# Optimization experiments

Measured on AMD Instinct MI355X. Metric: run time of the kernel, lower is better.

Reference implementation:

```python
import jax, jax.numpy as jnp
import numpy as np

TEMPERATURE = 0.5
EPS = 1e-8  # torch.nn.CosineSimilarity eps


def _l2norm(x):
    # torch cosine sim divides by max(||x||, eps) per vector
    n = jnp.sqrt(jnp.sum(x * x, axis=-1, keepdims=True))
    return x / jnp.maximum(n, EPS)


def setup_inputs() -> dict:
    key = jax.random.key(0)
    ka, kb = jax.random.split(key)
    batch_a = jax.random.normal(ka, (4096, 512), dtype=jnp.float32)
    batch_b = jax.random.normal(kb, (4096, 512), dtype=jnp.float32)
    return {"batch_a": batch_a, "batch_b": batch_b}


def reference(batch_a, batch_b):
    a = _l2norm(batch_a)  # [N, D]
    b = _l2norm(batch_b)
    inv_t = 1.0 / TEMPERATURE
    # cosine similarity via normalize + GEMM (same math as broadcast mul+reduce)
    sim11 = (a @ a.T) * inv_t  # [N, N]
    sim22 = (b @ b.T) * inv_t
    sim12 = (a @ b.T) * inv_t
    n = sim12.shape[-1]
    eye = jnp.eye(n, dtype=bool)
    neg_inf = jnp.float32(-jnp.inf)
    sim11 = jnp.where(eye, neg_inf, sim11)
    sim22 = jnp.where(eye, neg_inf, sim22)
    # logits: [[sim12, sim11], [sim22, sim12^T]] -> [2N, 2N]
    logits = jnp.concatenate(
        [jnp.concatenate([sim12, sim11], axis=-1),
         jnp.concatenate([sim22, sim12.T], axis=-1)],
        axis=-2,
    )
    targets = jnp.arange(2 * n)
    logp = jax.nn.log_softmax(logits, axis=-1)  # stable single pass
    loss = -jnp.mean(logp[jnp.arange(2 * n), targets])
    return loss
```

## Files before the change

### kernel.cpp

```cpp
#include <hip/hip_runtime.h>

#define NR 4096
#define DD 512
#define TWO_N 8192
#define MT2 32
#define NT2 528
#define CH2 66

using bf16x8 = __attribute__((ext_vector_type(8))) short;
using f32x4  = __attribute__((ext_vector_type(4))) float;

__device__ __forceinline__ unsigned short f2bf(float f) {
    union { float f; unsigned u; } v; v.f = f;
    unsigned r = v.u + 0x7fff + ((v.u >> 16) & 1);
    return (unsigned short)(r >> 16);
}

__global__ __launch_bounds__(256) void ntx_nrm_kernel(const float* __restrict__ A,
                                                      const float* __restrict__ B,
                                                      unsigned short* __restrict__ X,
                                                      float* __restrict__ d12,
                                                      float* __restrict__ S) {
    const int row = blockIdx.x;
    const int t = threadIdx.x;
    const int lane = t & 63, wid = t >> 6;

    if (t < 2) S[row * 2 + t] = 0.f;

    const float2 av = *(const float2*)(A + row * DD + 2 * t);
    const float2 bv = *(const float2*)(B + row * DD + 2 * t);
    float sa = av.x * av.x + av.y * av.y;
    float sb = bv.x * bv.x + bv.y * bv.y;
#pragma unroll
    for (int o = 32; o; o >>= 1) { sa += __shfl_down(sa, o); sb += __shfl_down(sb, o); }

    __shared__ float red[12];
    if (lane == 0) { red[wid] = sa; red[4 + wid] = sb; }
    __syncthreads();
    const float ta = red[0] + red[1] + red[2] + red[3];
    const float tb = red[4] + red[5] + red[6] + red[7];
    const float ra = 1.f / fmaxf(sqrtf(ta), 1e-8f);
    const float rb = 1.f / fmaxf(sqrtf(tb), 1e-8f);
    const float nax = av.x * ra, nay = av.y * ra;
    const float nbx = bv.x * rb, nby = bv.y * rb;

    *(unsigned*)(X + row * DD + 2 * t) =
        (unsigned)f2bf(nax) | ((unsigned)f2bf(nay) << 16);
    *(unsigned*)(X + (NR + row) * DD + 2 * t) =
        (unsigned)f2bf(nbx) | ((unsigned)f2bf(nby) << 16);

    float dt = nax * nbx + nay * nby;
#pragma unroll
    for (int o = 32; o; o >>= 1) dt += __shfl_down(dt, o);
    if (lane == 0) red[8 + wid] = dt;
    __syncthreads();
    if (t == 0) d12[row] = red[8] + red[9] + red[10] + red[11];
}

__global__ __launch_bounds__(512, 1) void ntx_gemm_lse_kernel(const unsigned short* __restrict__ X,
                                                              float* __restrict__ S) {
    const int bid = blockIdx.x;
    const int sid = (bid & 7) * CH2 + (bid >> 3);
    int u, v;
    if (sid < 448) {
        const int s = sid >> 4, loc = sid & 15;
        int U = 0;
        while (7 * (U + 1) - (U + 1) * U / 2 <= s) ++U;
        const int V = U + 1 + (s - (7 * U - U * (U - 1) / 2));
        u = U * 4 + (loc >> 2);
        v = V * 4 + (loc & 3);
    } else {
        const int s2 = sid - 448;
        const int U = s2 / 10, loc = s2 % 10;
        int lu = 0;
        while ((lu + 1) * 4 - (lu + 1) * lu / 2 <= loc) ++lu;
        const int lv = lu + (loc - (lu * 4 - lu * (lu - 1) / 2));
        u = U * 4 + lu;
        v = U * 4 + lv;
    }
    const bool fixedTile = (u == v);
    const int rowTile = u * 256, colTile = (v ^ 16) * 256;

    __shared__ unsigned short As[2][256 * 64];
    __shared__ unsigned short Bs[2][256 * 64];

    const int t = threadIdx.x;
    const int lane = t & 63, wid = t >> 6;
    const int waveM = wid >> 2, waveN = wid & 3;
    const int lr = lane & 15, grp = lane >> 4;
    const int r3 = lr & 7;

    f32x4 acc[8][4] = {};
    bf16x8 af[4][2];
    bf16x8 bf[4][2];

    const int srow = lane >> 3;
    const int scol = ((lane & 7) ^ srow) * 8;

    auto STAGE1 = [&](int sel, int kt, int q) {
        const int ci = wid * 4 + q;
        const int r  = ci * 8 + srow;
        const int lo = ci * 512 + lane * 8;
        __builtin_amdgcn_global_load_lds(
            (const __attribute__((address_space(1))) unsigned*)(X + (size_t)(rowTile + r) * DD + kt + scol),
            (__attribute__((address_space(3))) unsigned*)&As[sel][lo], 16, 0, 0);
        __builtin_amdgcn_global_load_lds(
            (const __attribute__((address_space(1))) unsigned*)(X + (size_t)((colTile + r) ^ NR) * DD + kt + scol),
            (__attribute__((address_space(3))) unsigned*)&Bs[sel][lo], 16, 0, 0);
    };

    auto LDA = [&](int sel, int mh) {
#pragma unroll
        for (int mm = 0; mm < 4; ++mm)
#pragma unroll
            for (int kk = 0; kk < 2; ++kk)
                af[mm][kk] = *(const bf16x8*)&As[sel][(waveM * 128 + (mh * 4 + mm) * 16 + lr) * 64 +
                                                      (((kk * 4 + grp) ^ r3) * 8)];
    };
    auto LDB = [&](int sel, int nh) {
#pragma unroll
        for (int nn = 0; nn < 2; ++nn)
#pragma unroll
            for (int kk = 0; kk < 2; ++kk)
                bf[nh * 2 + nn][kk] = *(const bf16x8*)&Bs[sel][(waveN * 64 + (nh * 2 + nn) * 16 + lr) * 64 +
                                                               (((kk * 4 + grp) ^ r3) * 8)];
    };
    auto QUAD = [&](int mh, int nh) {
        __builtin_amdgcn_s_setprio(1);
#pragma unroll
        for (int mm = 0; mm < 4; ++mm)
#pragma unroll
            for (int nn = 0; nn < 2; ++nn)
#pragma unroll
                for (int kk = 0; kk < 2; ++kk)
                    acc[mh * 4 + mm][nh * 2 + nn] = __builtin_amdgcn_mfma_f32_16x16x32_bf16(
                        af[mm][kk], bf[nh * 2 + nn][kk], acc[mh * 4 + mm][nh * 2 + nn], 0, 0, 0);
        __builtin_amdgcn_s_setprio(0);
    };

    STAGE1(0, 0, 0); STAGE1(0, 0, 1); STAGE1(0, 0, 2); STAGE1(0, 0, 3);
    asm volatile("s_waitcnt vmcnt(0)" ::: "memory");
    __builtin_amdgcn_s_barrier();

    for (int tt = 0; tt < 8; ++tt) {
        const int sel = tt & 1;
        const int kn = (tt + 1) * 64;
        LDA(sel, 0); LDB(sel, 0);
        if (tt < 7) { STAGE1(sel ^ 1, kn, 0); STAGE1(sel ^ 1, kn, 1); }
        __builtin_amdgcn_s_barrier();
        asm volatile("s_waitcnt lgkmcnt(0)" ::: "memory");
        __builtin_amdgcn_sched_barrier(0);
        QUAD(0, 0);
        __builtin_amdgcn_s_barrier();
        LDB(sel, 1);
        if (tt < 7) STAGE1(sel ^ 1, kn, 2);
        __builtin_amdgcn_s_barrier();
        asm volatile("s_waitcnt lgkmcnt(0)" ::: "memory");
        __builtin_amdgcn_sched_barrier(0);
        QUAD(0, 1);
        __builtin_amdgcn_s_barrier();
        LDA(sel, 1);
        if (tt < 7) STAGE1(sel ^ 1, kn, 3);
        __builtin_amdgcn_s_barrier();
        asm volatile("s_waitcnt lgkmcnt(0)" ::: "memory");
        __builtin_amdgcn_sched_barrier(0);
        QUAD(1, 1);
        __builtin_amdgcn_s_barrier();
        QUAD(1, 0);
        if (tt < 7) asm volatile("s_waitcnt vmcnt(0)" ::: "memory");
        __builtin_amdgcn_s_barrier();
    }

#pragma unroll
    for (int m = 0; m < 8; ++m)
#pragma unroll
        for (int n = 0; n < 4; ++n)
#pragma unroll
            for (int reg = 0; reg < 4; ++reg) {
                const int R = rowTile + waveM * 128 + m * 16 + grp * 4 + reg;
                const int C = colTile + waveN * 64 + n * 16 + lr;
                const bool masked = fixedTile && (C == (R ^ NR));
                acc[m][n][reg] = masked ? 0.f : __expf(acc[m][n][reg] * 2.0f);
            }

#pragma unroll
    for (int m = 0; m < 8; ++m)
#pragma unroll
        for (int reg = 0; reg < 4; ++reg) {
            float rs = acc[m][0][reg] + acc[m][1][reg] + acc[m][2][reg] + acc[m][3][reg];
            rs += __shfl_xor(rs, 1);
            rs += __shfl_xor(rs, 2);
            rs += __shfl_xor(rs, 4);
            rs += __shfl_xor(rs, 8);
            if (lr == 0) {
                const int R = rowTile + waveM * 128 + m * 16 + grp * 4 + reg;
                atomicAdd(&S[R], rs);
            }
        }

    if (!fixedTile) {
#pragma unroll
        for (int n = 0; n < 4; ++n) {
            float cs = 0.f;
#pragma unroll
            for (int m = 0; m < 8; ++m)
#pragma unroll
                for (int reg = 0; reg < 4; ++reg)
                    cs += acc[m][n][reg];
            cs += __shfl_xor(cs, 16);
            cs += __shfl_xor(cs, 32);
            if (grp == 0) {
                const int C = colTile + waveN * 64 + n * 16 + lr;
                atomicAdd(&S[C ^ NR], cs);
            }
        }
    }
}

__global__ __launch_bounds__(256) void ntx_loss_kernel(const float* __restrict__ S,
                                                       const float* __restrict__ d12,
                                                       float* __restrict__ out) {
    const int t = threadIdx.x;
    const int r = blockIdx.x * 256 + t;
    float a = __logf(S[r]) - 2.0f * d12[r & (NR - 1)];
    const int lane = t & 63, wid = t >> 6;
#pragma unroll
    for (int o = 32; o; o >>= 1) a += __shfl_down(a, o);
    __shared__ float red[4];
    if (lane == 0) red[wid] = a;
    __syncthreads();
    if (t == 0) atomicAdd(out, (red[0] + red[1] + red[2] + red[3]) * (1.f / (float)TWO_N));
}

extern "C" void kernel_launch(void* const* d_in, const int* in_sizes, int n_in,
                              void* d_out, int out_size, void* d_ws, size_t ws_size,
                              hipStream_t stream) {
    const float* A = (const float*)d_in[0];
    const float* B = (const float*)d_in[1];

    unsigned short* X = (unsigned short*)d_ws;
    float* S   = (float*)((char*)d_ws + (size_t)TWO_N * DD * 2);
    float* d12 = (float*)((char*)S + (size_t)TWO_N * 4);

    hipMemsetAsync(d_out, 0, sizeof(float), stream);

    ntx_nrm_kernel<<<NR, 256, 0, stream>>>(A, B, X, d12, S);

    ntx_gemm_lse_kernel<<<NT2, 512, 0, stream>>>(X, S);

    ntx_loss_kernel<<<TWO_N / 256, 256, 0, stream>>>(S, d12, (float*)d_out);
}
```

Before: 86.87 us.

## Switch GEMM mainloop to triple-buffered K=32 stages with deeper prefetch

The LDS staging in the fused GEMM+LSE kernel moves from double-buffered K=64 tiles to triple-buffered K=32 tiles. Global-to-LDS loads now run two stages ahead, gated by a partial vmcnt wait, and the XOR swizzle is redone for the narrower rows. The goal is to hide global load latency better and cut the per-iteration full vmcnt drain, at the cost of twice as many loop iterations and barriers.

```diff
diff --git a/kernel.cpp b/kernel.cpp
--- a/kernel.cpp
+++ b/kernel.cpp
@@ -81,25 +81,26 @@
     const bool fixedTile = (u == v);
     const int rowTile = u * 256, colTile = (v ^ 16) * 256;
 
-    __shared__ unsigned short As[2][256 * 64];
-    __shared__ unsigned short Bs[2][256 * 64];
+    __shared__ unsigned short As[3][256 * 32];
+    __shared__ unsigned short Bs[3][256 * 32];
 
     const int t = threadIdx.x;
     const int lane = t & 63, wid = t >> 6;
     const int waveM = wid >> 2, waveN = wid & 3;
     const int lr = lane & 15, grp = lane >> 4;
-    const int r3 = lr & 7;
+    const int swr = (lr >> 1) & 3;
+    const int kslot = (grp ^ swr) * 8;
 
     f32x4 acc[8][4] = {};
-    bf16x8 af[4][2];
-    bf16x8 bf[4][2];
-
-    const int srow = lane >> 3;
-    const int scol = ((lane & 7) ^ srow) * 8;
+    bf16x8 af[4];
+    bf16x8 bf[4];
+
+    const int srow = lane >> 2;
+    const int scol = ((lane & 3) ^ ((lane >> 3) & 3)) * 8;
 
     auto STAGE1 = [&](int sel, int kt, int q) {
-        const int ci = wid * 4 + q;
-        const int r  = ci * 8 + srow;
+        const int ci = wid * 2 + q;
+        const int r  = ci * 16 + srow;
         const int lo = ci * 512 + lane * 8;
         __builtin_amdgcn_global_load_lds(
             (const __attribute__((address_space(1))) unsigned*)(X + (size_t)(rowTile + r) * DD + kt + scol),
@@ -112,62 +113,49 @@
     auto LDA = [&](int sel, int mh) {
 #pragma unroll
         for (int mm = 0; mm < 4; ++mm)
-#pragma unroll
-            for (int kk = 0; kk < 2; ++kk)
-                af[mm][kk] = *(const bf16x8*)&As[sel][(waveM * 128 + (mh * 4 + mm) * 16 + lr) * 64 +
-                                                      (((kk * 4 + grp) ^ r3) * 8)];
-    };
-    auto LDB = [&](int sel, int nh) {
-#pragma unroll
-        for (int nn = 0; nn < 2; ++nn)
-#pragma unroll
-            for (int kk = 0; kk < 2; ++kk)
-                bf[nh * 2 + nn][kk] = *(const bf16x8*)&Bs[sel][(waveN * 64 + (nh * 2 + nn) * 16 + lr) * 64 +
-                                                               (((kk * 4 + grp) ^ r3) * 8)];
-    };
-    auto QUAD = [&](int mh, int nh) {
+            af[mm] = *(const bf16x8*)&As[sel][(waveM * 128 + (mh * 4 + mm) * 16 + lr) * 32 + kslot];
+    };
+    auto LDB = [&](int sel) {
+#pragma unroll
+        for (int n = 0; n < 4; ++n)
+            bf[n] = *(const bf16x8*)&Bs[sel][(waveN * 64 + n * 16 + lr) * 32 + kslot];
+    };
+    auto QUAD = [&](int mh) {
         __builtin_amdgcn_s_setprio(1);
 #pragma unroll
         for (int mm = 0; mm < 4; ++mm)
 #pragma unroll
-            for (int nn = 0; nn < 2; ++nn)
-#pragma unroll
-                for (int kk = 0; kk < 2; ++kk)
-                    acc[mh * 4 + mm][nh * 2 + nn] = __builtin_amdgcn_mfma_f32_16x16x32_bf16(
-                        af[mm][kk], bf[nh * 2 + nn][kk], acc[mh * 4 + mm][nh * 2 + nn], 0, 0, 0);
+            for (int n = 0; n < 4; ++n)
+                acc[mh * 4 + mm][n] = __builtin_amdgcn_mfma_f32_16x16x32_bf16(
+                    af[mm], bf[n], acc[mh * 4 + mm][n], 0, 0, 0);
         __builtin_amdgcn_s_setprio(0);
     };
 
-    STAGE1(0, 0, 0); STAGE1(0, 0, 1); STAGE1(0, 0, 2); STAGE1(0, 0, 3);
-    asm volatile("s_waitcnt vmcnt(0)" ::: "memory");
+    STAGE1(0, 0, 0);  STAGE1(0, 0, 1);
+    STAGE1(1, 32, 0); STAGE1(1, 32, 1);
+    asm volatile("s_waitcnt vmcnt(4)" ::: "memory");
     __builtin_amdgcn_s_barrier();
 
-    for (int tt = 0; tt < 8; ++tt) {
-        const int sel = tt & 1;
-        const int kn = (tt + 1) * 64;
-        LDA(sel, 0); LDB(sel, 0);
-        if (tt < 7) { STAGE1(sel ^ 1, kn, 0); STAGE1(sel ^ 1, kn, 1); }
+    for (int tt = 0; tt < 16; ++tt) {
+        const int sel = tt % 3;
+        const int nxt = (tt + 2) % 3;
+        const int kn = (tt + 2) * 32;
+        const bool st = (tt < 14);
+        LDB(sel); LDA(sel, 0);
+        if (st) STAGE1(nxt, kn, 0);
         __builtin_amdgcn_s_barrier();
         asm volatile("s_waitcnt lgkmcnt(0)" ::: "memory");
         __builtin_amdgcn_sched_barrier(0);
-        QUAD(0, 0);
-        __builtin_amdgcn_s_barrier();
-        LDB(sel, 1);
-        if (tt < 7) STAGE1(sel ^ 1, kn, 2);
+        QUAD(0);
+        __builtin_amdgcn_s_barrier();
+        LDA(sel, 1);
+        if (st) STAGE1(nxt, kn, 1);
         __builtin_amdgcn_s_barrier();
         asm volatile("s_waitcnt lgkmcnt(0)" ::: "memory");
         __builtin_amdgcn_sched_barrier(0);
-        QUAD(0, 1);
-        __builtin_amdgcn_s_barrier();
-        LDA(sel, 1);
-        if (tt < 7) STAGE1(sel ^ 1, kn, 3);
-        __builtin_amdgcn_s_barrier();
-        asm volatile("s_waitcnt lgkmcnt(0)" ::: "memory");
-        __builtin_amdgcn_sched_barrier(0);
-        QUAD(1, 1);
-        __builtin_amdgcn_s_barrier();
-        QUAD(1, 0);
-        if (tt < 7) asm volatile("s_waitcnt vmcnt(0)" ::: "memory");
+        QUAD(1);
+        if (tt < 14)       asm volatile("s_waitcnt vmcnt(4)" ::: "memory");
+        else if (tt == 14) asm volatile("s_waitcnt vmcnt(0)" ::: "memory");
         __builtin_amdgcn_s_barrier();
     }
 
@@ -242,7 +230,7 @@
     float* S   = (float*)((char*)d_ws + (size_t)TWO_N * DD * 2);
     float* d12 = (float*)((char*)S + (size_t)TWO_N * 4);
 
-    hipMemsetAsync(d_out, 0, sizeof(float), stream);
+    (void)hipMemsetAsync(d_out, 0, sizeof(float), stream);
 
     ntx_nrm_kernel<<<NR, 256, 0, stream>>>(A, B, X, d12, S);
 
```

New measurement: 90.35 us. 4.0% more time.
